# Kernel optimization log

Measured on AMD Instinct MI355X. Metric: run time of the kernel, lower is better.

The kernel has to match this reference:

```python
import jax, jax.numpy as jnp
import numpy as np

EPS = 1e-5

def _ln(x, g, b):
    m = jnp.mean(x, axis=-1, keepdims=True)
    v = jnp.var(x, axis=-1, keepdims=True)
    return (x - m) / jnp.sqrt(v + EPS) * g + b

def _lin(x, w, b):
    # torch-style weight [out, in]
    return x @ w.T + b

def _mlp(x, w1, b1, w2, b2):
    # Mlp: Linear -> exact GELU -> Linear (dropout=0)
    return _lin(jax.nn.gelu(_lin(x, w1, b1), approximate=False), w2, b2)

def setup_inputs() -> dict:
    B, C, H, W = 2, 256, 64, 64
    key = jax.random.key(0)
    ks = jax.random.split(key, 32)
    s = 0.02  # param init scale keeps attention logits in a sane range
    d = {
        'center_fea': jax.random.normal(ks[0], (B, C, H, W), jnp.float32),
        'wh_fea':     jax.random.normal(ks[1], (B, C, H, W), jnp.float32),
        'cls_fea':    jax.random.normal(ks[2], (B, C, H, W), jnp.float32),
        'mix_w': jax.random.normal(ks[3], (C, 3 * C), jnp.float32) * s,
        'mix_b': jnp.zeros((C,), jnp.float32),
        'ln_g': jnp.ones((C,), jnp.float32),
        'ln_b': jnp.zeros((C,), jnp.float32),
        'q1_w': jax.random.normal(ks[4], (C, C), jnp.float32) * s,
        'q1_b': jnp.zeros((C,), jnp.float32),
        'q2_w': jax.random.normal(ks[5], (C, C), jnp.float32) * s,
        'q2_b': jnp.zeros((C,), jnp.float32),
        'q3_w': jax.random.normal(ks[6], (C, C), jnp.float32) * s,
        'q3_b': jnp.zeros((C,), jnp.float32),
        'k_w': jax.random.normal(ks[7], (C, C), jnp.float32) * s,
        'k_b': jnp.zeros((C,), jnp.float32),
        'v_w': jax.random.normal(ks[8], (C, C), jnp.float32) * s,
        'v_b': jnp.zeros((C,), jnp.float32),
        'cmlp_w1': jax.random.normal(ks[9], (C, C), jnp.float32) * s,
        'cmlp_b1': jnp.zeros((C,), jnp.float32),
        'cmlp_w2': jax.random.normal(ks[10], (C, C), jnp.float32) * s,
        'cmlp_b2': jnp.zeros((C,), jnp.float32),
        'wmlp_w1': jax.random.normal(ks[11], (C, C), jnp.float32) * s,
        'wmlp_b1': jnp.zeros((C,), jnp.float32),
        'wmlp_w2': jax.random.normal(ks[12], (C, C), jnp.float32) * s,
        'wmlp_b2': jnp.zeros((C,), jnp.float32),
        'clsmlp_w1': jax.random.normal(ks[13], (C, C), jnp.float32) * s,
        'clsmlp_b1': jnp.zeros((C,), jnp.float32),
        'clsmlp_w2': jax.random.normal(ks[14], (C, C), jnp.float32) * s,
        'clsmlp_b2': jnp.zeros((C,), jnp.float32),
    }
    return d

def reference(center_fea, wh_fea, cls_fea, mix_w, mix_b, ln_g, ln_b,
              q1_w, q1_b, q2_w, q2_b, q3_w, q3_b, k_w, k_b, v_w, v_b,
              cmlp_w1, cmlp_b1, cmlp_w2, cmlp_b2,
              wmlp_w1, wmlp_b1, wmlp_w2, wmlp_b2,
              clsmlp_w1, clsmlp_b1, clsmlp_w2, clsmlp_b2):
    b, c, h, w = center_fea.shape
    # 1x1 conv mix over concatenated channels [b, 3c, h, w] -> [b, c, h, w]
    cat = jnp.concatenate([center_fea, wh_fea, cls_fea], axis=1)
    mix = jnp.einsum('oc,bchw->bohw', mix_w, cat) + mix_b[None, :, None, None]

    tok = lambda x: x.reshape(b, c, h * w).transpose(0, 2, 1)  # [b, N, c]
    cf, wf, clf, mf = tok(center_fea), tok(wh_fea), tok(cls_fea), tok(mix)

    ct, wt, clt, mt = _ln(cf, ln_g, ln_b), _ln(wf, ln_g, ln_b), _ln(clf, ln_g, ln_b), _ln(mf, ln_g, ln_b)

    kf = _lin(mt, k_w, k_b)  # shared K
    vf = _lin(mt, v_w, v_b)  # shared V

    def attend(q):
        score = jax.nn.softmax(jnp.einsum('bnd,bmd->bnm', q, kf), axis=-1)  # [b, N, N]
        return jnp.einsum('bnm,bmd->bnd', score, vf)

    cf  = _ln(cf  + attend(_lin(ct,  q1_w, q1_b)), ln_g, ln_b)
    wf  = _ln(wf  + attend(_lin(wt,  q2_w, q2_b)), ln_g, ln_b)
    clf = _ln(clf + attend(_lin(clt, q3_w, q3_b)), ln_g, ln_b)

    cf  = _ln(cf  + _mlp(cf,  cmlp_w1, cmlp_b1, cmlp_w2, cmlp_b2), ln_g, ln_b)
    wf  = _ln(wf  + _mlp(wf,  wmlp_w1, wmlp_b1, wmlp_w2, wmlp_b2), ln_g, ln_b)
    clf = _ln(clf + _mlp(clf, clsmlp_w1, clsmlp_b1, clsmlp_w2, clsmlp_b2), ln_g, ln_b)

    untok = lambda x: x.transpose(0, 2, 1).reshape(b, c, h, w)
    return (untok(cf), untok(wf), untok(clf))
```

## Files before the change

kernel.cpp:

```cpp
#include <hip/hip_runtime.h>
#include <hip/hip_bf16.h>
#include <math.h>

typedef unsigned int   u32;
typedef unsigned short u16;
typedef float floatx4 __attribute__((ext_vector_type(4)));
typedef short bf16x8  __attribute__((ext_vector_type(8)));

#define MFMA16(a,b,c) __builtin_amdgcn_mfma_f32_16x16x32_bf16((a),(b),(c),0,0,0)

static __device__ __forceinline__ float bfbits2f(u16 h){
    return __uint_as_float(((u32)h) << 16);
}
static __device__ __forceinline__ u16 f2bfbits(float f){
    u32 u = __float_as_uint(f);
    u32 r = (u + 0x7fffu + ((u >> 16) & 1u)) >> 16;
    return (u16)r;
}
static __device__ __forceinline__ bool sniff_bf16(const void* ln_g){
    return ((const u32*)ln_g)[0] == 0x3f803f80u;
}

typedef __attribute__((address_space(1))) const unsigned int gas_u32;
typedef __attribute__((address_space(3))) unsigned int las_u32;
static __device__ __forceinline__ void gl_lds16(const void* g, void* l){
    __builtin_amdgcn_global_load_lds((gas_u32*)g, (las_u32*)l, 16, 0, 0);
}

#define DPPF(v, ctrl) __uint_as_float((u32)__builtin_amdgcn_update_dpp( \
        (int)__float_as_uint(v), (int)__float_as_uint(v), (ctrl), 0xf, 0xf, true))

static __device__ __forceinline__ float red16_max(float v){
    v = fmaxf(v, DPPF(v, 0xB1));
    v = fmaxf(v, DPPF(v, 0x4E));
    v = fmaxf(v, DPPF(v, 0x141));
    v = fmaxf(v, DPPF(v, 0x140));
    return v;
}
static __device__ __forceinline__ float red16_sum(float v){
    v += DPPF(v, 0xB1);
    v += DPPF(v, 0x4E);
    v += DPPF(v, 0x141);
    v += DPPF(v, 0x140);
    return v;
}

struct PackJob { const void* src; void* dst; int n; int mode; };
struct PackParams { PackJob jobs[26]; const void* lng; };

__global__ __launch_bounds__(256) void k_pack(PackParams p){
    bool isb = sniff_bf16(p.lng);
    PackJob j = p.jobs[blockIdx.y];
    for (int i = blockIdx.x * 256 + threadIdx.x; i < j.n; i += 256 * 256){
        float v = isb ? bfbits2f(((const u16*)j.src)[i]) : ((const float*)j.src)[i];
        if (j.mode == 0) ((u16*)j.dst)[i]  = f2bfbits(v);
        else             ((float*)j.dst)[i] = v;
    }
}

struct FtParams { const void* src[3]; u16* dst[3]; const void* lng; };

__global__ __launch_bounds__(256) void k_feat_t(FtParams p){
    bool isb = sniff_bf16(p.lng);
    int z = blockIdx.z; int si = z >> 1; int b = z & 1;
    const void* src = p.src[si]; u16* dst = p.dst[si];
    int n0 = blockIdx.x * 64, c0 = blockIdx.y * 64;
    __shared__ float tile[64][65];
    int t = threadIdx.x; int tx = t & 63; int ty = t >> 6;
    #pragma unroll
    for (int pp = 0; pp < 16; ++pp){
        int cl = ty + pp * 4;
        size_t off = ((size_t)b * 256 + c0 + cl) * 4096 + n0 + tx;
        float v = isb ? bfbits2f(((const u16*)src)[off]) : ((const float*)src)[off];
        tile[cl][tx] = v;
    }
    __syncthreads();
    #pragma unroll
    for (int pp = 0; pp < 16; ++pp){
        int nl = ty + pp * 4; int cl = tx;
        dst[((size_t)b * 4096 + n0 + nl) * 256 + c0 + cl] = f2bfbits(tile[cl][nl]);
    }
}

struct GemmJob { const u16* A0; const u16* A1; const u16* A2;
                 const u16* W; const float* bias; const u16* res; u16* out; };
struct GemmParams { GemmJob jobs[5]; int K; int op; };

__global__ __launch_bounds__(256, 4) void k_gemm(GemmParams p){
    GemmJob j = p.jobs[blockIdx.z];
    int m0 = blockIdx.x * 64, n0 = blockIdx.y * 64;
    __shared__ __align__(16) u16 As[2][64][64];
    __shared__ __align__(16) u16 Bs[2][64][64];
    int t = threadIdx.x;
    int wave = t >> 6, lane = t & 63, l15 = lane & 15, quad = lane >> 4;
    int mh = (wave & 1) * 32, nh = (wave >> 1) * 32;
    int key = l15 & 7;

    auto stage = [&](int bi, int k0){
        const u16* Ap = (k0 < 256) ? j.A0 : (k0 < 512 ? j.A1 : j.A2);
        int koff = k0 & 255;
        #pragma unroll
        for (int i = 0; i < 2; ++i){
            int rq = wave * 2 + i;
            int r  = rq * 8 + (lane >> 3);
            int gs = (lane & 7) ^ (r & 7);
            gl_lds16(Ap  + (size_t)(m0 + r) * 256 + koff + gs * 8, &As[bi][rq * 8][0]);
            gl_lds16(j.W + (size_t)(n0 + r) * p.K + k0   + gs * 8, &Bs[bi][rq * 8][0]);
        }
    };

    floatx4 acc[2][2];
    #pragma unroll
    for (int a = 0; a < 2; ++a)
        #pragma unroll
        for (int bq = 0; bq < 2; ++bq) acc[a][bq] = (floatx4){0.f,0.f,0.f,0.f};

    stage(0, 0);
    __syncthreads();
    int nk = p.K >> 6, buf = 0;

    for (int ks = 0; ks < nk; ++ks){
        if (ks + 1 < nk) stage(buf ^ 1, (ks + 1) * 64);
        #pragma unroll
        for (int kc = 0; kc < 2; ++kc){
            int gsel = ((kc * 4 + quad) ^ key) * 8;
            bf16x8 a0 = *(const bf16x8*)&As[buf][mh +      l15][gsel];
            bf16x8 a1 = *(const bf16x8*)&As[buf][mh + 16 + l15][gsel];
            bf16x8 b0 = *(const bf16x8*)&Bs[buf][nh +      l15][gsel];
            bf16x8 b1 = *(const bf16x8*)&Bs[buf][nh + 16 + l15][gsel];
            acc[0][0] = MFMA16(a0, b0, acc[0][0]);
            acc[0][1] = MFMA16(a0, b1, acc[0][1]);
            acc[1][0] = MFMA16(a1, b0, acc[1][0]);
            acc[1][1] = MFMA16(a1, b1, acc[1][1]);
        }
        __syncthreads();
        buf ^= 1;
    }

    #pragma unroll
    for (int mb = 0; mb < 2; ++mb)
        #pragma unroll
        for (int nb = 0; nb < 2; ++nb){
            int col = n0 + nh + nb * 16 + l15;
            float bias = j.bias[col];
            #pragma unroll
            for (int rg = 0; rg < 4; ++rg){
                int row = m0 + mh + mb * 16 + quad * 4 + rg;
                float v = acc[mb][nb][rg] + bias;
                if (p.op == 1)      v = 0.5f * v * (1.0f + erff(v * 0.70710678118f));
                else if (p.op == 2) v += bfbits2f(j.res[(size_t)row * 256 + col]);
                j.out[(size_t)row * 256 + col] = f2bfbits(v);
            }
        }
}

struct LnJob { const u16* src; u16* dst; };
struct LnParams { LnJob jobs[4]; const float* g; const float* b; };

__global__ __launch_bounds__(256, 4) void k_ln(LnParams p){
    LnJob j = p.jobs[blockIdx.y];
    int g16 = threadIdx.x >> 4, l = threadIdx.x & 15;
    size_t tok = (size_t)blockIdx.x * 16 + g16;
    const u16* row = j.src + tok * 256 + l * 16;
    uint4 ra = *(const uint4*)(row);
    uint4 rb = *(const uint4*)(row + 8);
    u32 wv[8] = {ra.x, ra.y, ra.z, ra.w, rb.x, rb.y, rb.z, rb.w};
    float va[16];
    float s1 = 0.f, s2 = 0.f;
    #pragma unroll
    for (int i = 0; i < 8; ++i){
        float a = bfbits2f((u16)(wv[i] & 0xffffu));
        float c = bfbits2f((u16)(wv[i] >> 16));
        va[2*i] = a; va[2*i+1] = c;
        s1 += a + c; s2 += a*a + c*c;
    }
    s1 = red16_sum(s1); s2 = red16_sum(s2);
    float mean = s1 * (1.f/256.f);
    float var  = s2 * (1.f/256.f) - mean * mean;
    float rstd = rsqrtf(var + 1e-5f);
    int c0 = l * 16;
    u32 ow[8];
    #pragma unroll
    for (int i = 0; i < 8; ++i){
        float x0 = (va[2*i]   - mean) * rstd * p.g[c0 + 2*i]     + p.b[c0 + 2*i];
        float x1 = (va[2*i+1] - mean) * rstd * p.g[c0 + 2*i + 1] + p.b[c0 + 2*i + 1];
        ow[i] = (u32)f2bfbits(x0) | ((u32)f2bfbits(x1) << 16);
    }
    u16* dst = j.dst + tok * 256 + c0;
    *(uint4*)(dst)     = (uint4){ow[0], ow[1], ow[2], ow[3]};
    *(uint4*)(dst + 8) = (uint4){ow[4], ow[5], ow[6], ow[7]};
}

__global__ __launch_bounds__(256, 4) void k_vt(const u16* __restrict__ Vf, u16* __restrict__ Vt){
    int b = blockIdx.z;
    int n0 = blockIdx.x * 64, c0 = blockIdx.y * 64;
    __shared__ u16 tile[64][66];
    int t = threadIdx.x; int tx = t & 63; int ty = t >> 6;
    #pragma unroll
    for (int pp = 0; pp < 16; ++pp){
        int nl = ty + pp * 4;
        tile[nl][tx] = Vf[((size_t)b * 4096 + n0 + nl) * 256 + c0 + tx];
    }
    __syncthreads();
    #pragma unroll
    for (int pp = 0; pp < 16; ++pp){
        int cl = ty + pp * 4; int nl = tx;
        Vt[((size_t)b * 256 + c0 + cl) * 4096 + n0 + nl] = tile[nl][cl];
    }
}

struct FlashParams {
    const u16* Q[3]; const u16* K; const u16* Vt;
    const u16* Res[3]; u16* Out[3];
    const float* g; const float* b;
};

__global__ __launch_bounds__(256, 2) void k_flash(FlashParams p){
    int s = blockIdx.y >> 1, b = blockIdx.y & 1;
    int m0 = blockIdx.x * 64;
    const u16* Q   = p.Q[s]   + (size_t)b * 4096 * 256;
    const u16* Kf  = p.K      + (size_t)b * 4096 * 256;
    const u16* Vtg = p.Vt     + (size_t)b * 256 * 4096;
    const u16* Res = p.Res[s] + (size_t)b * 4096 * 256;
    u16*       Out = p.Out[s] + (size_t)b * 4096 * 256;

    __shared__ __align__(16) u16 Kb[2][32][256];
    __shared__ __align__(16) u16 Vb[2][256][32];
    __shared__ __align__(16) u16 Pl[4][16][40];

    int t = threadIdx.x, wave = t >> 6, lane = t & 63, l15 = lane & 15, quad = lane >> 4;

    auto stage = [&](int bi, int kv0){
        #pragma unroll
        for (int m = 0; m < 4; ++m){
            int q = wave * 4 + m;
            int r0 = q * 2 + (lane >> 5);
            int gg = (lane & 31) ^ (r0 & 7);
            gl_lds16(Kf + (size_t)(kv0 + r0) * 256 + gg * 8, &Kb[bi][q * 2][0]);
        }
        #pragma unroll
        for (int m = 0; m < 4; ++m){
            int q = wave * 4 + m;
            int d = q * 16 + (lane >> 2);
            int gg = (lane & 3) ^ ((d >> 1) & 3);
            gl_lds16(Vtg + (size_t)d * 4096 + kv0 + gg * 8, &Vb[bi][q * 16][0]);
        }
    };

    stage(0, 0);

    bf16x8 qf[8];
    {
        const u16* qrow = Q + (size_t)(m0 + wave * 16 + l15) * 256 + quad * 8;
        #pragma unroll
        for (int kc = 0; kc < 8; ++kc) qf[kc] = *(const bf16x8*)(qrow + kc * 32);
    }
    floatx4 o[16];
    #pragma unroll
    for (int i = 0; i < 16; ++i) o[i] = (floatx4){0.f,0.f,0.f,0.f};
    float mrow[4] = {-INFINITY,-INFINITY,-INFINITY,-INFINITY};
    float lsum[4] = {0.f,0.f,0.f,0.f};

    __syncthreads();
    int buf = 0;

    for (int ch = 0; ch < 128; ++ch){
        if (ch < 127) stage(buf ^ 1, (ch + 1) * 32);

        floatx4 sa[2];
        __builtin_amdgcn_s_setprio(1);
        #pragma unroll
        for (int sub = 0; sub < 2; ++sub){
            int row = sub * 16 + l15;
            floatx4 a0 = (floatx4){0.f,0.f,0.f,0.f};
            floatx4 a1 = (floatx4){0.f,0.f,0.f,0.f};
            #pragma unroll
            for (int kc = 0; kc < 4; ++kc){
                bf16x8 kb0 = *(const bf16x8*)&Kb[buf][row][((((2*kc  ) * 4 + quad) ^ (row & 7))) * 8];
                bf16x8 kb1 = *(const bf16x8*)&Kb[buf][row][((((2*kc+1) * 4 + quad) ^ (row & 7))) * 8];
                a0 = MFMA16(qf[2*kc  ], kb0, a0);
                a1 = MFMA16(qf[2*kc+1], kb1, a1);
            }
            sa[sub] = a0 + a1;
        }
        __builtin_amdgcn_s_setprio(0);

        float al[4]; int grow = 0;
        #pragma unroll
        for (int rg = 0; rg < 4; ++rg){
            float m1 = red16_max(fmaxf(sa[0][rg], sa[1][rg]));
            grow |= (m1 > mrow[rg]) ? 1 : 0;
            float mn = fmaxf(mrow[rg], m1);
            al[rg] = __expf(mrow[rg] - mn);
            mrow[rg] = mn;
        }
        #pragma unroll
        for (int rg = 0; rg < 4; ++rg){
            float p0 = __expf(sa[0][rg] - mrow[rg]);
            float p1 = __expf(sa[1][rg] - mrow[rg]);
            sa[0][rg] = p0; sa[1][rg] = p1;
            lsum[rg] = lsum[rg] * al[rg] + (p0 + p1);
        }

        #pragma unroll
        for (int sub = 0; sub < 2; ++sub)
            #pragma unroll
            for (int rg = 0; rg < 4; ++rg)
                Pl[wave][quad * 4 + rg][sub * 16 + l15] = f2bfbits(sa[sub][rg]);

        if (__any(grow)){
            #pragma unroll
            for (int dc = 0; dc < 16; ++dc)
                #pragma unroll
                for (int rg = 0; rg < 4; ++rg) o[dc][rg] *= al[rg];
        }

        asm volatile("s_waitcnt lgkmcnt(0)" ::: "memory");
        __builtin_amdgcn_sched_barrier(0);

        bf16x8 pa = *(const bf16x8*)&Pl[wave][l15][quad * 8];
        __builtin_amdgcn_s_setprio(1);
        #pragma unroll
        for (int dc = 0; dc < 16; ++dc){
            int row = dc * 16 + l15;
            bf16x8 vb = *(const bf16x8*)&Vb[buf][row][((quad ^ ((row >> 1) & 3))) * 8];
            o[dc] = MFMA16(pa, vb, o[dc]);
        }
        __builtin_amdgcn_s_setprio(0);

        __syncthreads();
        buf ^= 1;
    }

    float inv[4];
    #pragma unroll
    for (int rg = 0; rg < 4; ++rg) inv[rg] = 1.0f / red16_sum(lsum[rg]);
    float s1[4] = {0.f,0.f,0.f,0.f}, s2[4] = {0.f,0.f,0.f,0.f};
    #pragma unroll
    for (int dc = 0; dc < 16; ++dc)
        #pragma unroll
        for (int rg = 0; rg < 4; ++rg){
            int row = m0 + wave * 16 + quad * 4 + rg;
            float v = o[dc][rg] * inv[rg] + bfbits2f(Res[(size_t)row * 256 + dc * 16 + l15]);
            o[dc][rg] = v;
            s1[rg] += v; s2[rg] += v * v;
        }
    #pragma unroll
    for (int rg = 0; rg < 4; ++rg){
        float mean = red16_sum(s1[rg]) * (1.f/256.f);
        float q2   = red16_sum(s2[rg]);
        float var  = q2 * (1.f/256.f) - mean * mean;
        s1[rg] = mean; s2[rg] = rsqrtf(var + 1e-5f);
    }
    #pragma unroll
    for (int dc = 0; dc < 16; ++dc){
        int c = dc * 16 + l15;
        float gv = p.g[c], bv = p.b[c];
        #pragma unroll
        for (int rg = 0; rg < 4; ++rg){
            int row = m0 + wave * 16 + quad * 4 + rg;
            Out[(size_t)row * 256 + c] = f2bfbits((o[dc][rg] - s1[rg]) * s2[rg] * gv + bv);
        }
    }
}

struct OutTParams { const u16* F[3]; void* out; const void* lng; };

__global__ __launch_bounds__(256, 4) void k_out_t(OutTParams p){
    bool isb = sniff_bf16(p.lng);
    int z = blockIdx.z; int s = z >> 1; int b = z & 1;
    const u16* F = p.F[s];
    int n0 = blockIdx.x * 64, c0 = blockIdx.y * 64;
    __shared__ u16 tile[64][66];
    int t = threadIdx.x; int tx = t & 63; int ty = t >> 6;
    #pragma unroll
    for (int pp = 0; pp < 16; ++pp){
        int nl = ty + pp * 4;
        tile[nl][tx] = F[((size_t)b * 4096 + n0 + nl) * 256 + c0 + tx];
    }
    __syncthreads();
    size_t obase = ((size_t)s * 2 + b) * 256 * 4096;
    #pragma unroll
    for (int pp = 0; pp < 16; ++pp){
        int cl = ty + pp * 4; int nl = tx;
        u16 raw = tile[nl][cl];
        size_t off = obase + (size_t)(c0 + cl) * 4096 + n0 + nl;
        if (isb) ((u16*)p.out)[off]   = raw;
        else     ((float*)p.out)[off] = bfbits2f(raw);
    }
}

extern "C" void kernel_launch(void* const* d_in, const int* in_sizes, int n_in,
                              void* d_out, int out_size, void* d_ws, size_t ws_size,
                              hipStream_t stream) {
    (void)in_sizes; (void)n_in; (void)out_size; (void)ws_size;
    const size_t SLOT = (size_t)2 * 4096 * 256;
    u16* ws = (u16*)d_ws;
    auto slot = [&](int i){ return ws + (size_t)i * SLOT; };

    u16 *Tc = slot(0),  *Tw = slot(1),  *Tcl = slot(2),  *Tm = slot(3);
    u16 *Lc = slot(4),  *Lw = slot(5),  *Lcl = slot(6),  *Lm = slot(7);
    u16 *Q1 = slot(8),  *Q2 = slot(9),  *Q3  = slot(10);
    u16 *Kf = slot(11), *Vf = slot(12), *Vt  = slot(13);
    u16 *Yc = slot(14), *Yw = slot(15), *Ycl = slot(16);
    u16 *Hc = Q1, *Hw = Q2, *Hcl = Q3;
    u16 *Zc = Lc, *Zw = Lw, *Zcl = Lcl;
    u16 *Fc = Kf, *Fw = Vf, *Fcl = Vt;

    u16* wbase = slot(17);
    u16 *mixw = wbase;
    u16 *q1w = wbase + 196608, *q2w = q1w + 65536, *q3w = q2w + 65536;
    u16 *kw  = q3w + 65536,    *vw  = kw  + 65536;
    u16 *cw1 = vw  + 65536, *cw2 = cw1 + 65536, *ww1 = cw2 + 65536,
        *ww2 = ww1 + 65536, *clw1 = ww2 + 65536, *clw2 = clw1 + 65536;
    float* pbase = (float*)(wbase + 1048576);
    float *mixb = pbase,        *lng = pbase+256,  *lnb = pbase+512,
          *q1b = pbase+768,  *q2b = pbase+1024, *q3b = pbase+1280,
          *kb  = pbase+1536, *vb  = pbase+1792,
          *cb1 = pbase+2048, *cb2 = pbase+2304, *wb1 = pbase+2560,
          *wb2 = pbase+2816, *clb1= pbase+3072, *clb2= pbase+3328;

    {
        PackParams pp;
        const int widx[12] = {3,7,9,11,13,15,17,19,21,23,25,27};
        u16* wdst[12] = {mixw,q1w,q2w,q3w,kw,vw,cw1,cw2,ww1,ww2,clw1,clw2};
        for (int i = 0; i < 12; ++i)
            pp.jobs[i] = PackJob{ d_in[widx[i]], wdst[i], (i==0?196608:65536), 0 };
        const int pidx[14] = {4,5,6,8,10,12,14,16,18,20,22,24,26,28};
        float* pdst[14] = {mixb,lng,lnb,q1b,q2b,q3b,kb,vb,cb1,cb2,wb1,wb2,clb1,clb2};
        for (int i = 0; i < 14; ++i)
            pp.jobs[12+i] = PackJob{ d_in[pidx[i]], pdst[i], 256, 1 };
        pp.lng = d_in[5];
        hipLaunchKernelGGL(k_pack, dim3(256, 26), dim3(256), 0, stream, pp);
    }
    {
        FtParams fp;
        fp.src[0] = d_in[0]; fp.src[1] = d_in[1]; fp.src[2] = d_in[2];
        fp.dst[0] = Tc; fp.dst[1] = Tw; fp.dst[2] = Tcl;
        fp.lng = d_in[5];
        hipLaunchKernelGGL(k_feat_t, dim3(64, 4, 6), dim3(256), 0, stream, fp);
    }
    {
        GemmParams gp; gp.K = 768; gp.op = 0;
        gp.jobs[0] = GemmJob{ Tc, Tw, Tcl, mixw, mixb, nullptr, Tm };
        hipLaunchKernelGGL(k_gemm, dim3(128, 4, 1), dim3(256), 0, stream, gp);
    }
    {
        LnParams lp; lp.g = lng; lp.b = lnb;
        lp.jobs[0] = LnJob{Tc, Lc}; lp.jobs[1] = LnJob{Tw, Lw};
        lp.jobs[2] = LnJob{Tcl, Lcl}; lp.jobs[3] = LnJob{Tm, Lm};
        hipLaunchKernelGGL(k_ln, dim3(512, 4), dim3(256), 0, stream, lp);
    }
    {
        GemmParams gp; gp.K = 256; gp.op = 0;
        gp.jobs[0] = GemmJob{ Lc,  nullptr, nullptr, q1w, q1b, nullptr, Q1 };
        gp.jobs[1] = GemmJob{ Lw,  nullptr, nullptr, q2w, q2b, nullptr, Q2 };
        gp.jobs[2] = GemmJob{ Lcl, nullptr, nullptr, q3w, q3b, nullptr, Q3 };
        gp.jobs[3] = GemmJob{ Lm,  nullptr, nullptr, kw,  kb,  nullptr, Kf };
        gp.jobs[4] = GemmJob{ Lm,  nullptr, nullptr, vw,  vb,  nullptr, Vf };
        hipLaunchKernelGGL(k_gemm, dim3(128, 4, 5), dim3(256), 0, stream, gp);
    }
    hipLaunchKernelGGL(k_vt, dim3(64, 4, 2), dim3(256), 0, stream, Vf, Vt);
    {
        FlashParams fp;
        fp.Q[0] = Q1; fp.Q[1] = Q2; fp.Q[2] = Q3;
        fp.K = Kf; fp.Vt = Vt;
        fp.Res[0] = Tc; fp.Res[1] = Tw; fp.Res[2] = Tcl;
        fp.Out[0] = Yc; fp.Out[1] = Yw; fp.Out[2] = Ycl;
        fp.g = lng; fp.b = lnb;
        hipLaunchKernelGGL(k_flash, dim3(64, 6), dim3(256), 0, stream, fp);
    }
    {
        GemmParams gp; gp.K = 256; gp.op = 1;
        gp.jobs[0] = GemmJob{ Yc,  nullptr, nullptr, cw1,  cb1,  nullptr, Hc };
        gp.jobs[1] = GemmJob{ Yw,  nullptr, nullptr, ww1,  wb1,  nullptr, Hw };
        gp.jobs[2] = GemmJob{ Ycl, nullptr, nullptr, clw1, clb1, nullptr, Hcl };
        hipLaunchKernelGGL(k_gemm, dim3(128, 4, 3), dim3(256), 0, stream, gp);
    }
    {
        GemmParams gp; gp.K = 256; gp.op = 2;
        gp.jobs[0] = GemmJob{ Hc,  nullptr, nullptr, cw2,  cb2,  Yc,  Zc };
        gp.jobs[1] = GemmJob{ Hw,  nullptr, nullptr, ww2,  wb2,  Yw,  Zw };
        gp.jobs[2] = GemmJob{ Hcl, nullptr, nullptr, clw2, clb2, Ycl, Zcl };
        hipLaunchKernelGGL(k_gemm, dim3(128, 4, 3), dim3(256), 0, stream, gp);
    }
    {
        LnParams lp; lp.g = lng; lp.b = lnb;
        lp.jobs[0] = LnJob{Zc, Fc}; lp.jobs[1] = LnJob{Zw, Fw};
        lp.jobs[2] = LnJob{Zcl, Fcl}; lp.jobs[3] = LnJob{Zc, Fc};
        hipLaunchKernelGGL(k_ln, dim3(512, 3), dim3(256), 0, stream, lp);
    }
    {
        OutTParams op;
        op.F[0] = Fc; op.F[1] = Fw; op.F[2] = Fcl;
        op.out = d_out; op.lng = d_in[5];
        hipLaunchKernelGGL(k_out_t, dim3(64, 4, 6), dim3(256), 0, stream, op);
    }
}
```

Baseline: 426.2 us.

## Fuse V transpose into GEMM, fuse final LN with output transpose, widen flash tile

The V projection GEMM now also writes a transposed copy of its tile through shared memory, which removes the separate k_vt transpose kernel. The final LayerNorm and the output transpose are merged into one k_ln_out kernel, cutting an intermediate round trip through global memory. The flash attention kernel now handles 128 query rows per block, two 16-row groups per wave, so each K/V tile staged in LDS feeds twice as many MFMAs. In exchange it drops setprio hints and goes to one block per CU, with higher register pressure and fewer blocks (192) on the device.

```diff
diff --git a/kernel.cpp b/kernel.cpp
--- a/kernel.cpp
+++ b/kernel.cpp
@@ -83,7 +83,8 @@
 }
 
 struct GemmJob { const u16* A0; const u16* A1; const u16* A2;
-                 const u16* W; const float* bias; const u16* res; u16* out; };
+                 const u16* W; const float* bias; const u16* res;
+                 u16* out; u16* outT; };
 struct GemmParams { GemmJob jobs[5]; int K; int op; };
 
 __global__ __launch_bounds__(256, 4) void k_gemm(GemmParams p){
@@ -137,6 +138,7 @@
         buf ^= 1;
     }
 
+    u16* scratch = (u16*)&As[0][0][0];
     #pragma unroll
     for (int mb = 0; mb < 2; ++mb)
         #pragma unroll
@@ -149,9 +151,22 @@
                 float v = acc[mb][nb][rg] + bias;
                 if (p.op == 1)      v = 0.5f * v * (1.0f + erff(v * 0.70710678118f));
                 else if (p.op == 2) v += bfbits2f(j.res[(size_t)row * 256 + col]);
-                j.out[(size_t)row * 256 + col] = f2bfbits(v);
-            }
-        }
+                u16 bits = f2bfbits(v);
+                j.out[(size_t)row * 256 + col] = bits;
+                if (j.outT)
+                    scratch[(nh + nb * 16 + l15) * 72 + (mh + mb * 16 + quad * 4 + rg)] = bits;
+            }
+        }
+    if (j.outT){
+        __syncthreads();
+        int b2 = m0 >> 12, tok0 = m0 & 4095;
+        #pragma unroll
+        for (int pp2 = 0; pp2 < 16; ++pp2){
+            int cl = (t >> 6) + pp2 * 4, tx = t & 63;
+            j.outT[(size_t)b2 * 1048576 + (size_t)(n0 + cl) * 4096 + tok0 + tx]
+                = scratch[cl * 72 + tx];
+        }
+    }
 }
 
 struct LnJob { const u16* src; u16* dst; };
@@ -191,21 +206,54 @@
     *(uint4*)(dst + 8) = (uint4){ow[4], ow[5], ow[6], ow[7]};
 }
 
-__global__ __launch_bounds__(256, 4) void k_vt(const u16* __restrict__ Vf, u16* __restrict__ Vt){
-    int b = blockIdx.z;
-    int n0 = blockIdx.x * 64, c0 = blockIdx.y * 64;
-    __shared__ u16 tile[64][66];
-    int t = threadIdx.x; int tx = t & 63; int ty = t >> 6;
-    #pragma unroll
-    for (int pp = 0; pp < 16; ++pp){
-        int nl = ty + pp * 4;
-        tile[nl][tx] = Vf[((size_t)b * 4096 + n0 + nl) * 256 + c0 + tx];
+struct LnOutParams { const u16* Z[3]; void* out; const float* g; const float* b; const void* lng; };
+
+__global__ __launch_bounds__(256, 4) void k_ln_out(LnOutParams p){
+    bool isb = sniff_bf16(p.lng);
+    int y = blockIdx.y; int s = y >> 1, b = y & 1;
+    const u16* Z = p.Z[s] + (size_t)b * 4096 * 256;
+    int tok0 = blockIdx.x * 64;
+    __shared__ u16 tile[64][258];
+    int t = threadIdx.x, g16 = t >> 4, l = t & 15;
+    #pragma unroll
+    for (int pass = 0; pass < 4; ++pass){
+        int tl = pass * 16 + g16;
+        const u16* row = Z + (size_t)(tok0 + tl) * 256 + l * 16;
+        uint4 ra = *(const uint4*)(row);
+        uint4 rb = *(const uint4*)(row + 8);
+        u32 wv[8] = {ra.x, ra.y, ra.z, ra.w, rb.x, rb.y, rb.z, rb.w};
+        float va[16];
+        float s1 = 0.f, s2 = 0.f;
+        #pragma unroll
+        for (int i = 0; i < 8; ++i){
+            float a = bfbits2f((u16)(wv[i] & 0xffffu));
+            float c = bfbits2f((u16)(wv[i] >> 16));
+            va[2*i] = a; va[2*i+1] = c;
+            s1 += a + c; s2 += a*a + c*c;
+        }
+        s1 = red16_sum(s1); s2 = red16_sum(s2);
+        float mean = s1 * (1.f/256.f);
+        float var  = s2 * (1.f/256.f) - mean * mean;
+        float rstd = rsqrtf(var + 1e-5f);
+        int c0 = l * 16;
+        u32* drow = (u32*)&tile[tl][c0];
+        #pragma unroll
+        for (int i = 0; i < 8; ++i){
+            float x0 = (va[2*i]   - mean) * rstd * p.g[c0 + 2*i]     + p.b[c0 + 2*i];
+            float x1 = (va[2*i+1] - mean) * rstd * p.g[c0 + 2*i + 1] + p.b[c0 + 2*i + 1];
+            drow[i] = (u32)f2bfbits(x0) | ((u32)f2bfbits(x1) << 16);
+        }
     }
     __syncthreads();
-    #pragma unroll
-    for (int pp = 0; pp < 16; ++pp){
-        int cl = ty + pp * 4; int nl = tx;
-        Vt[((size_t)b * 256 + c0 + cl) * 4096 + n0 + nl] = tile[nl][cl];
+    size_t obase = ((size_t)s * 2 + b) * 256 * 4096;
+    int cq = t >> 6, tl2 = t & 63;
+    #pragma unroll
+    for (int pp = 0; pp < 64; ++pp){
+        int c = pp * 4 + cq;
+        u16 raw = tile[tl2][c];
+        size_t off = obase + (size_t)c * 4096 + tok0 + tl2;
+        if (isb) ((u16*)p.out)[off]   = raw;
+        else     ((float*)p.out)[off] = bfbits2f(raw);
     }
 }
 
@@ -215,9 +263,9 @@
     const float* g; const float* b;
 };
 
-__global__ __launch_bounds__(256, 2) void k_flash(FlashParams p){
+__global__ __launch_bounds__(256, 1) void k_flash(FlashParams p){
     int s = blockIdx.y >> 1, b = blockIdx.y & 1;
-    int m0 = blockIdx.x * 64;
+    int m0 = blockIdx.x * 128;
     const u16* Q   = p.Q[s]   + (size_t)b * 4096 * 256;
     const u16* Kf  = p.K      + (size_t)b * 4096 * 256;
     const u16* Vtg = p.Vt     + (size_t)b * 256 * 4096;
@@ -226,7 +274,7 @@
 
     __shared__ __align__(16) u16 Kb[2][32][256];
     __shared__ __align__(16) u16 Vb[2][256][32];
-    __shared__ __align__(16) u16 Pl[4][16][40];
+    __shared__ __align__(16) u16 Pl[4][32][40];
 
     int t = threadIdx.x, wave = t >> 6, lane = t & 63, l15 = lane & 15, quad = lane >> 4;
 
@@ -249,17 +297,23 @@
 
     stage(0, 0);
 
-    bf16x8 qf[8];
-    {
-        const u16* qrow = Q + (size_t)(m0 + wave * 16 + l15) * 256 + quad * 8;
-        #pragma unroll
-        for (int kc = 0; kc < 8; ++kc) qf[kc] = *(const bf16x8*)(qrow + kc * 32);
-    }
-    floatx4 o[16];
-    #pragma unroll
-    for (int i = 0; i < 16; ++i) o[i] = (floatx4){0.f,0.f,0.f,0.f};
-    float mrow[4] = {-INFINITY,-INFINITY,-INFINITY,-INFINITY};
-    float lsum[4] = {0.f,0.f,0.f,0.f};
+    bf16x8 qf[2][8];
+    #pragma unroll
+    for (int h = 0; h < 2; ++h){
+        const u16* qrow = Q + (size_t)(m0 + wave * 32 + h * 16 + l15) * 256 + quad * 8;
+        #pragma unroll
+        for (int kc = 0; kc < 8; ++kc) qf[h][kc] = *(const bf16x8*)(qrow + kc * 32);
+    }
+    floatx4 o[2][16];
+    #pragma unroll
+    for (int h = 0; h < 2; ++h)
+        #pragma unroll
+        for (int i = 0; i < 16; ++i) o[h][i] = (floatx4){0.f,0.f,0.f,0.f};
+    float mrow[2][4], lsum[2][4];
+    #pragma unroll
+    for (int h = 0; h < 2; ++h)
+        #pragma unroll
+        for (int rg = 0; rg < 4; ++rg){ mrow[h][rg] = -INFINITY; lsum[h][rg] = 0.f; }
 
     __syncthreads();
     int buf = 0;
@@ -267,126 +321,106 @@
     for (int ch = 0; ch < 128; ++ch){
         if (ch < 127) stage(buf ^ 1, (ch + 1) * 32);
 
-        floatx4 sa[2];
-        __builtin_amdgcn_s_setprio(1);
+        floatx4 sa[2][2];
         #pragma unroll
         for (int sub = 0; sub < 2; ++sub){
             int row = sub * 16 + l15;
-            floatx4 a0 = (floatx4){0.f,0.f,0.f,0.f};
-            floatx4 a1 = (floatx4){0.f,0.f,0.f,0.f};
+            floatx4 e0 = (floatx4){0.f,0.f,0.f,0.f}, e1 = (floatx4){0.f,0.f,0.f,0.f};
+            floatx4 f0 = (floatx4){0.f,0.f,0.f,0.f}, f1 = (floatx4){0.f,0.f,0.f,0.f};
             #pragma unroll
             for (int kc = 0; kc < 4; ++kc){
                 bf16x8 kb0 = *(const bf16x8*)&Kb[buf][row][((((2*kc  ) * 4 + quad) ^ (row & 7))) * 8];
                 bf16x8 kb1 = *(const bf16x8*)&Kb[buf][row][((((2*kc+1) * 4 + quad) ^ (row & 7))) * 8];
-                a0 = MFMA16(qf[2*kc  ], kb0, a0);
-                a1 = MFMA16(qf[2*kc+1], kb1, a1);
-            }
-            sa[sub] = a0 + a1;
-        }
-        __builtin_amdgcn_s_setprio(0);
-
-        float al[4]; int grow = 0;
-        #pragma unroll
-        for (int rg = 0; rg < 4; ++rg){
-            float m1 = red16_max(fmaxf(sa[0][rg], sa[1][rg]));
-            grow |= (m1 > mrow[rg]) ? 1 : 0;
-            float mn = fmaxf(mrow[rg], m1);
-            al[rg] = __expf(mrow[rg] - mn);
-            mrow[rg] = mn;
-        }
-        #pragma unroll
-        for (int rg = 0; rg < 4; ++rg){
-            float p0 = __expf(sa[0][rg] - mrow[rg]);
-            float p1 = __expf(sa[1][rg] - mrow[rg]);
-            sa[0][rg] = p0; sa[1][rg] = p1;
-            lsum[rg] = lsum[rg] * al[rg] + (p0 + p1);
-        }
-
-        #pragma unroll
-        for (int sub = 0; sub < 2; ++sub)
-            #pragma unroll
-            for (int rg = 0; rg < 4; ++rg)
-                Pl[wave][quad * 4 + rg][sub * 16 + l15] = f2bfbits(sa[sub][rg]);
-
-        if (__any(grow)){
-            #pragma unroll
-            for (int dc = 0; dc < 16; ++dc)
+                e0 = MFMA16(qf[0][2*kc  ], kb0, e0);
+                e1 = MFMA16(qf[0][2*kc+1], kb1, e1);
+                f0 = MFMA16(qf[1][2*kc  ], kb0, f0);
+                f1 = MFMA16(qf[1][2*kc+1], kb1, f1);
+            }
+            sa[0][sub] = e0 + e1;
+            sa[1][sub] = f0 + f1;
+        }
+
+        #pragma unroll
+        for (int h = 0; h < 2; ++h){
+            float al[4]; int grow = 0;
+            #pragma unroll
+            for (int rg = 0; rg < 4; ++rg){
+                float m1 = red16_max(fmaxf(sa[h][0][rg], sa[h][1][rg]));
+                grow |= (m1 > mrow[h][rg]) ? 1 : 0;
+                float mn = fmaxf(mrow[h][rg], m1);
+                al[rg] = __expf(mrow[h][rg] - mn);
+                mrow[h][rg] = mn;
+            }
+            #pragma unroll
+            for (int rg = 0; rg < 4; ++rg){
+                float p0 = __expf(sa[h][0][rg] - mrow[h][rg]);
+                float p1 = __expf(sa[h][1][rg] - mrow[h][rg]);
+                sa[h][0][rg] = p0; sa[h][1][rg] = p1;
+                lsum[h][rg] = lsum[h][rg] * al[rg] + (p0 + p1);
+            }
+            #pragma unroll
+            for (int sub = 0; sub < 2; ++sub)
                 #pragma unroll
-                for (int rg = 0; rg < 4; ++rg) o[dc][rg] *= al[rg];
+                for (int rg = 0; rg < 4; ++rg)
+                    Pl[wave][h * 16 + quad * 4 + rg][sub * 16 + l15] = f2bfbits(sa[h][sub][rg]);
+            if (__any(grow)){
+                #pragma unroll
+                for (int dc = 0; dc < 16; ++dc)
+                    #pragma unroll
+                    for (int rg = 0; rg < 4; ++rg) o[h][dc][rg] *= al[rg];
+            }
         }
 
         asm volatile("s_waitcnt lgkmcnt(0)" ::: "memory");
         __builtin_amdgcn_sched_barrier(0);
 
-        bf16x8 pa = *(const bf16x8*)&Pl[wave][l15][quad * 8];
-        __builtin_amdgcn_s_setprio(1);
+        bf16x8 pa[2];
+        pa[0] = *(const bf16x8*)&Pl[wave][     l15][quad * 8];
+        pa[1] = *(const bf16x8*)&Pl[wave][16 + l15][quad * 8];
         #pragma unroll
         for (int dc = 0; dc < 16; ++dc){
             int row = dc * 16 + l15;
             bf16x8 vb = *(const bf16x8*)&Vb[buf][row][((quad ^ ((row >> 1) & 3))) * 8];
-            o[dc] = MFMA16(pa, vb, o[dc]);
-        }
-        __builtin_amdgcn_s_setprio(0);
+            o[0][dc] = MFMA16(pa[0], vb, o[0][dc]);
+            o[1][dc] = MFMA16(pa[1], vb, o[1][dc]);
+        }
 
         __syncthreads();
         buf ^= 1;
     }
 
-    float inv[4];
-    #pragma unroll
-    for (int rg = 0; rg < 4; ++rg) inv[rg] = 1.0f / red16_sum(lsum[rg]);
-    float s1[4] = {0.f,0.f,0.f,0.f}, s2[4] = {0.f,0.f,0.f,0.f};
-    #pragma unroll
-    for (int dc = 0; dc < 16; ++dc)
+    #pragma unroll
+    for (int h = 0; h < 2; ++h){
+        float inv[4];
+        #pragma unroll
+        for (int rg = 0; rg < 4; ++rg) inv[rg] = 1.0f / red16_sum(lsum[h][rg]);
+        float s1[4] = {0.f,0.f,0.f,0.f}, s2[4] = {0.f,0.f,0.f,0.f};
+        #pragma unroll
+        for (int dc = 0; dc < 16; ++dc)
+            #pragma unroll
+            for (int rg = 0; rg < 4; ++rg){
+                int row = m0 + wave * 32 + h * 16 + quad * 4 + rg;
+                float v = o[h][dc][rg] * inv[rg] + bfbits2f(Res[(size_t)row * 256 + dc * 16 + l15]);
+                o[h][dc][rg] = v;
+                s1[rg] += v; s2[rg] += v * v;
+            }
         #pragma unroll
         for (int rg = 0; rg < 4; ++rg){
-            int row = m0 + wave * 16 + quad * 4 + rg;
-            float v = o[dc][rg] * inv[rg] + bfbits2f(Res[(size_t)row * 256 + dc * 16 + l15]);
-            o[dc][rg] = v;
-            s1[rg] += v; s2[rg] += v * v;
-        }
-    #pragma unroll
-    for (int rg = 0; rg < 4; ++rg){
-        float mean = red16_sum(s1[rg]) * (1.f/256.f);
-        float q2   = red16_sum(s2[rg]);
-        float var  = q2 * (1.f/256.f) - mean * mean;
-        s1[rg] = mean; s2[rg] = rsqrtf(var + 1e-5f);
-    }
-    #pragma unroll
-    for (int dc = 0; dc < 16; ++dc){
-        int c = dc * 16 + l15;
-        float gv = p.g[c], bv = p.b[c];
-        #pragma unroll
-        for (int rg = 0; rg < 4; ++rg){
-            int row = m0 + wave * 16 + quad * 4 + rg;
-            Out[(size_t)row * 256 + c] = f2bfbits((o[dc][rg] - s1[rg]) * s2[rg] * gv + bv);
-        }
-    }
-}
-
-struct OutTParams { const u16* F[3]; void* out; const void* lng; };
-
-__global__ __launch_bounds__(256, 4) void k_out_t(OutTParams p){
-    bool isb = sniff_bf16(p.lng);
-    int z = blockIdx.z; int s = z >> 1; int b = z & 1;
-    const u16* F = p.F[s];
-    int n0 = blockIdx.x * 64, c0 = blockIdx.y * 64;
-    __shared__ u16 tile[64][66];
-    int t = threadIdx.x; int tx = t & 63; int ty = t >> 6;
-    #pragma unroll
-    for (int pp = 0; pp < 16; ++pp){
-        int nl = ty + pp * 4;
-        tile[nl][tx] = F[((size_t)b * 4096 + n0 + nl) * 256 + c0 + tx];
-    }
-    __syncthreads();
-    size_t obase = ((size_t)s * 2 + b) * 256 * 4096;
-    #pragma unroll
-    for (int pp = 0; pp < 16; ++pp){
-        int cl = ty + pp * 4; int nl = tx;
-        u16 raw = tile[nl][cl];
-        size_t off = obase + (size_t)(c0 + cl) * 4096 + n0 + nl;
-        if (isb) ((u16*)p.out)[off]   = raw;
-        else     ((float*)p.out)[off] = bfbits2f(raw);
+            float mean = red16_sum(s1[rg]) * (1.f/256.f);
+            float q2   = red16_sum(s2[rg]);
+            float var  = q2 * (1.f/256.f) - mean * mean;
+            s1[rg] = mean; s2[rg] = rsqrtf(var + 1e-5f);
+        }
+        #pragma unroll
+        for (int dc = 0; dc < 16; ++dc){
+            int c = dc * 16 + l15;
+            float gv = p.g[c], bv = p.b[c];
+            #pragma unroll
+            for (int rg = 0; rg < 4; ++rg){
+                int row = m0 + wave * 32 + h * 16 + quad * 4 + rg;
+                Out[(size_t)row * 256 + c] = f2bfbits((o[h][dc][rg] - s1[rg]) * s2[rg] * gv + bv);
+            }
+        }
     }
 }
 
@@ -405,7 +439,6 @@
     u16 *Yc = slot(14), *Yw = slot(15), *Ycl = slot(16);
     u16 *Hc = Q1, *Hw = Q2, *Hcl = Q3;
     u16 *Zc = Lc, *Zw = Lw, *Zcl = Lcl;
-    u16 *Fc = Kf, *Fw = Vf, *Fcl = Vt;
 
     u16* wbase = slot(17);
     u16 *mixw = wbase;
@@ -442,7 +475,7 @@
     }
     {
         GemmParams gp; gp.K = 768; gp.op = 0;
-        gp.jobs[0] = GemmJob{ Tc, Tw, Tcl, mixw, mixb, nullptr, Tm };
+        gp.jobs[0] = GemmJob{ Tc, Tw, Tcl, mixw, mixb, nullptr, Tm, nullptr };
         hipLaunchKernelGGL(k_gemm, dim3(128, 4, 1), dim3(256), 0, stream, gp);
     }
     {
@@ -453,14 +486,13 @@
     }
     {
         GemmParams gp; gp.K = 256; gp.op = 0;
-        gp.jobs[0] = GemmJob{ Lc,  nullptr, nullptr, q1w, q1b, nullptr, Q1 };
-        gp.jobs[1] = GemmJob{ Lw,  nullptr, nullptr, q2w, q2b, nullptr, Q2 };
-        gp.jobs[2] = GemmJob{ Lcl, nullptr, nullptr, q3w, q3b, nullptr, Q3 };
-        gp.jobs[3] = GemmJob{ Lm,  nullptr, nullptr, kw,  kb,  nullptr, Kf };
-        gp.jobs[4] = GemmJob{ Lm,  nullptr, nullptr, vw,  vb,  nullptr, Vf };
+        gp.jobs[0] = GemmJob{ Lc,  nullptr, nullptr, q1w, q1b, nullptr, Q1, nullptr };
+        gp.jobs[1] = GemmJob{ Lw,  nullptr, nullptr, q2w, q2b, nullptr, Q2, nullptr };
+        gp.jobs[2] = GemmJob{ Lcl, nullptr, nullptr, q3w, q3b, nullptr, Q3, nullptr };
+        gp.jobs[3] = GemmJob{ Lm,  nullptr, nullptr, kw,  kb,  nullptr, Kf, nullptr };
+        gp.jobs[4] = GemmJob{ Lm,  nullptr, nullptr, vw,  vb,  nullptr, Vf, Vt };
         hipLaunchKernelGGL(k_gemm, dim3(128, 4, 5), dim3(256), 0, stream, gp);
     }
-    hipLaunchKernelGGL(k_vt, dim3(64, 4, 2), dim3(256), 0, stream, Vf, Vt);
     {
         FlashParams fp;
         fp.Q[0] = Q1; fp.Q[1] = Q2; fp.Q[2] = Q3;
@@ -468,32 +500,26 @@
         fp.Res[0] = Tc; fp.Res[1] = Tw; fp.Res[2] = Tcl;
         fp.Out[0] = Yc; fp.Out[1] = Yw; fp.Out[2] = Ycl;
         fp.g = lng; fp.b = lnb;
-        hipLaunchKernelGGL(k_flash, dim3(64, 6), dim3(256), 0, stream, fp);
+        hipLaunchKernelGGL(k_flash, dim3(32, 6), dim3(256), 0, stream, fp);
     }
     {
         GemmParams gp; gp.K = 256; gp.op = 1;
-        gp.jobs[0] = GemmJob{ Yc,  nullptr, nullptr, cw1,  cb1,  nullptr, Hc };
-        gp.jobs[1] = GemmJob{ Yw,  nullptr, nullptr, ww1,  wb1,  nullptr, Hw };
-        gp.jobs[2] = GemmJob{ Ycl, nullptr, nullptr, clw1, clb1, nullptr, Hcl };
+        gp.jobs[0] = GemmJob{ Yc,  nullptr, nullptr, cw1,  cb1,  nullptr, Hc,  nullptr };
+        gp.jobs[1] = GemmJob{ Yw,  nullptr, nullptr, ww1,  wb1,  nullptr, Hw,  nullptr };
+        gp.jobs[2] = GemmJob{ Ycl, nullptr, nullptr, clw1, clb1, nullptr, Hcl, nullptr };
         hipLaunchKernelGGL(k_gemm, dim3(128, 4, 3), dim3(256), 0, stream, gp);
     }
     {
         GemmParams gp; gp.K = 256; gp.op = 2;
-        gp.jobs[0] = GemmJob{ Hc,  nullptr, nullptr, cw2,  cb2,  Yc,  Zc };
-        gp.jobs[1] = GemmJob{ Hw,  nullptr, nullptr, ww2,  wb2,  Yw,  Zw };
-        gp.jobs[2] = GemmJob{ Hcl, nullptr, nullptr, clw2, clb2, Ycl, Zcl };
+        gp.jobs[0] = GemmJob{ Hc,  nullptr, nullptr, cw2,  cb2,  Yc,  Zc,  nullptr };
+        gp.jobs[1] = GemmJob{ Hw,  nullptr, nullptr, ww2,  wb2,  Yw,  Zw,  nullptr };
+        gp.jobs[2] = GemmJob{ Hcl, nullptr, nullptr, clw2, clb2, Ycl, Zcl, nullptr };
         hipLaunchKernelGGL(k_gemm, dim3(128, 4, 3), dim3(256), 0, stream, gp);
     }
     {
-        LnParams lp; lp.g = lng; lp.b = lnb;
-        lp.jobs[0] = LnJob{Zc, Fc}; lp.jobs[1] = LnJob{Zw, Fw};
-        lp.jobs[2] = LnJob{Zcl, Fcl}; lp.jobs[3] = LnJob{Zc, Fc};
-        hipLaunchKernelGGL(k_ln, dim3(512, 3), dim3(256), 0, stream, lp);
-    }
-    {
-        OutTParams op;
-        op.F[0] = Fc; op.F[1] = Fw; op.F[2] = Fcl;
-        op.out = d_out; op.lng = d_in[5];
-        hipLaunchKernelGGL(k_out_t, dim3(64, 4, 6), dim3(256), 0, stream, op);
-    }
-}
+        LnOutParams lo;
+        lo.Z[0] = Zc; lo.Z[1] = Zw; lo.Z[2] = Zcl;
+        lo.out = d_out; lo.g = lng; lo.b = lnb; lo.lng = d_in[5];
+        hipLaunchKernelGGL(k_ln_out, dim3(64, 6), dim3(256), 0, stream, lo);
+    }
+}
```

New measurement: 495.3 us. 1.16x slower.
